# Kernel optimization log

Measured on AMD Instinct MI355X. Metric: run time of the kernel, lower is better.

Reference implementation:

```python
import jax, jax.numpy as jnp
import numpy as np
import math

B, S, D, H = 2, 2048, 1024, 16
HD = D // H  # head_dim = 64
NEG = -1.0e9


def _xavier(key, shape, gain):
    fan_in, fan_out = shape[1], shape[0]
    bound = gain * math.sqrt(6.0 / (fan_in + fan_out))
    return jax.random.uniform(key, shape, jnp.float32, -bound, bound)


def setup_inputs() -> dict:
    key = jax.random.key(0)
    ks = jax.random.split(key, 7)
    gain = 1.0 / math.sqrt(2.0)
    q = jax.random.normal(ks[0], (B, S, D), jnp.float32)
    pad_mask = jax.random.randint(ks[1], (B, S), 0, 2) > 0  # True = masked key
    # ensure not all keys masked per row
    pad_mask = pad_mask.at[:, 0].set(False)
    Wq = _xavier(ks[2], (D, D), gain)
    Wk = _xavier(ks[3], (D, D), gain)
    Wv = _xavier(ks[4], (D, D), gain)
    Wo = _xavier(ks[5], (D, D), gain)
    bk = jax.random.normal(ks[6], (4, D), jnp.float32) * 0.02
    return {"q": q, "pad_mask": pad_mask,
            "Wq": Wq, "bq": bk[0], "Wk": Wk, "bk": bk[1],
            "Wv": Wv, "bv": bk[2], "Wo": Wo, "bo": bk[3]}


def reference(q, pad_mask, Wq, bq, Wk, bk, Wv, bv, Wo, bo):
    # Self-attention: k = v = q (k, v args are None in this config)
    x = q
    # torch Linear: y = x @ W.T + b
    qh = (x @ Wq.T + bq).reshape(B, S, H, HD).transpose(0, 2, 1, 3)  # [B,H,S,HD]
    kh = (x @ Wk.T + bk).reshape(B, S, H, HD).transpose(0, 2, 1, 3)
    vh = (x @ Wv.T + bv).reshape(B, S, H, HD).transpose(0, 2, 1, 3)

    scores = jnp.einsum('bhqd,bhkd->bhqk', qh, kh) / math.sqrt(HD)  # [B,H,S,S]
    causal = jnp.triu(jnp.ones((S, S), bool), k=1)                  # [S,S]
    scores = jnp.where(causal[None, None], NEG, scores)
    scores = jnp.where(pad_mask[:, None, None, :], NEG, scores)

    probs = jax.nn.softmax(scores, axis=-1)
    out = jnp.einsum('bhqk,bhkd->bhqd', probs, vh)                  # [B,H,S,HD]
    out = out.transpose(0, 2, 1, 3).reshape(B, S, D)
    return out @ Wo.T + bo
```

## Files before the change

kernel.cpp:

```cpp
#include <hip/hip_runtime.h>
#include <hip/hip_bf16.h>

#define BB 2
#define SS 2048
#define DD 1024
#define HH 16
#define HD 64
#define MM (BB * SS)
#define NQKV 3072

typedef __attribute__((ext_vector_type(8))) short short8;
typedef __attribute__((ext_vector_type(4))) short s16x4;
typedef __attribute__((ext_vector_type(4))) float floatx4;
typedef __attribute__((ext_vector_type(4))) float f32x4;
using bf16 = __hip_bfloat16;

__device__ __forceinline__ float b2f(bf16 x) { return __bfloat162float(x); }
__device__ __forceinline__ short f2bs(float x) {
    bf16 h = __float2bfloat16(x);
    return *reinterpret_cast<short*>(&h);
}
__device__ __forceinline__ float bs2f(short s) {
    bf16 h; *reinterpret_cast<short*>(&h) = s; return __bfloat162float(h);
}

__device__ __forceinline__ int lds_off(int row, int chunk) {
    return row * 64 + ((chunk ^ (row & 7)) * 8);
}

#define GL16(gp, lp)                                                        \
    __builtin_amdgcn_global_load_lds(                                       \
        (const __attribute__((address_space(1))) void*)(gp),                \
        (__attribute__((address_space(3))) void*)(lp), 16, 0, 0)

#define N_WCAT (NQKV * DD / 4)
#define N_X    (MM * DD / 4)
#define N_WOB  (DD * DD / 4)

__global__ __launch_bounds__(256) void convert_all(
    const float* __restrict__ Wq, const float* __restrict__ Wk,
    const float* __restrict__ Wv, const float* __restrict__ X,
    const float* __restrict__ Wo,
    short* __restrict__ wcat, short* __restrict__ xb, short* wob)
{
    const int total = N_WCAT + N_X + (wob ? N_WOB : 0);
    const int stride = gridDim.x * blockDim.x;
    for (int i = blockIdx.x * blockDim.x + threadIdx.x; i < total; i += stride) {
        f32x4 v; short* dp;
        if (i < N_WCAT) {
            const int e = i * 4;
            const int z = e >> 20;
            const int off = e & 0xFFFFF;
            const float* src = (z == 0) ? Wq : (z == 1) ? Wk : Wv;
            v = *(const f32x4*)(src + off);
            dp = wcat + e;
        } else if (i < N_WCAT + N_X) {
            const int e = (i - N_WCAT) * 4;
            v = *(const f32x4*)(X + e);
            dp = xb + e;
        } else {
            const int e = (i - N_WCAT - N_X) * 4;
            v = *(const f32x4*)(Wo + e);
            dp = wob + e;
        }
        s16x4 o; o[0] = f2bs(v[0]); o[1] = f2bs(v[1]); o[2] = f2bs(v[2]); o[3] = f2bs(v[3]);
        *(s16x4*)dp = o;
    }
}

__global__ __launch_bounds__(256) void convert_w(
    const float* __restrict__ W, short* __restrict__ dst)
{
    const int stride = gridDim.x * blockDim.x;
    for (int i = blockIdx.x * blockDim.x + threadIdx.x; i < DD * DD / 4; i += stride) {
        f32x4 v = *(const f32x4*)(W + i * 4);
        s16x4 o; o[0] = f2bs(v[0]); o[1] = f2bs(v[1]); o[2] = f2bs(v[2]); o[3] = f2bs(v[3]);
        *(s16x4*)(dst + i * 4) = o;
    }
}

__global__ __launch_bounds__(256, 6) void qkv_gemm2(
    const short* __restrict__ Xb, const short* __restrict__ Wcat,
    const float* __restrict__ bq, const float* __restrict__ bk, const float* __restrict__ bv,
    bf16* __restrict__ outQ, bf16* __restrict__ outK, bf16* __restrict__ outV)
{
    __shared__ short As[128 * 64];
    __shared__ short Bs[64 * 64];

    const int tid  = threadIdx.x;
    const int lane = tid & 63;
    const int wave = tid >> 6;
    const int wm   = wave & 1;
    const int wn   = wave >> 1;
    const int g    = lane >> 4;
    const int fr   = lane & 15;

    const int m0 = blockIdx.x * 128;
    const int n0 = blockIdx.y * 64;

    const int l8  = lane >> 3;
    const int sch = (lane & 7) ^ l8;
    const short* agl = Xb   + (size_t)(m0 + l8) * DD + sch * 8;
    const short* bgl = Wcat + (size_t)(n0 + l8) * DD + sch * 8;

    floatx4 acc[4][2];
#pragma unroll
    for (int i = 0; i < 4; ++i)
#pragma unroll
        for (int j = 0; j < 2; ++j) acc[i][j] = (floatx4){0.f, 0.f, 0.f, 0.f};

    for (int kb = 0; kb < DD; kb += 64) {
        __syncthreads();
#pragma unroll
        for (int j = 0; j < 4; ++j) {
            const int r = wave * 32 + j * 8;
            GL16(agl + (size_t)r * DD + kb, &As[r * 64]);
        }
#pragma unroll
        for (int j = 0; j < 2; ++j) {
            const int r = wave * 16 + j * 8;
            GL16(bgl + (size_t)r * DD + kb, &Bs[r * 64]);
        }
        __syncthreads();

#pragma unroll
        for (int kk = 0; kk < 2; ++kk) {
            const int kc = kk * 4 + g;
            short8 af[4], bf[2];
#pragma unroll
            for (int t = 0; t < 4; ++t)
                af[t] = *(const short8*)&As[lds_off(wm * 64 + t * 16 + fr, kc)];
#pragma unroll
            for (int u = 0; u < 2; ++u)
                bf[u] = *(const short8*)&Bs[lds_off(wn * 32 + u * 16 + fr, kc)];
#pragma unroll
            for (int mt = 0; mt < 4; ++mt)
#pragma unroll
                for (int nt = 0; nt < 2; ++nt)
                    acc[mt][nt] = __builtin_amdgcn_mfma_f32_16x16x32_bf16(
                        af[mt], bf[nt], acc[mt][nt], 0, 0, 0);
        }
    }

#pragma unroll
    for (int nt = 0; nt < 2; ++nt) {
        const int n  = n0 + wn * 32 + nt * 16 + fr;
        const int z  = n >> 10;
        const int nn = n & 1023;
        const int h_ = nn >> 6;
        const int d_ = nn & 63;
        const float biasv = ((z == 0) ? bq : (z == 1) ? bk : bv)[nn];
        bf16* outp = (z == 0) ? outQ : (z == 1) ? outK : outV;
#pragma unroll
        for (int mt = 0; mt < 4; ++mt) {
#pragma unroll
            for (int reg = 0; reg < 4; ++reg) {
                const int m  = m0 + wm * 64 + mt * 16 + g * 4 + reg;
                const int b_ = m >> 11;
                const int s_ = m & (SS - 1);
                const float v = acc[mt][nt][reg] + biasv;
                size_t off;
                if (z == 2) off = ((size_t)((b_ * HH + h_) * HD + d_)) * SS + s_;
                else        off = ((size_t)((b_ * HH + h_) * SS + s_)) * HD + d_;
                outp[off] = __float2bfloat16(v);
            }
        }
    }
}

__global__ __launch_bounds__(256, 6) void o_gemm2(
    const short* __restrict__ A, const short* __restrict__ Wob,
    const float* __restrict__ bias, float* __restrict__ out)
{
    __shared__ short As[128 * 64];
    __shared__ short Bs[64 * 64];

    const int tid  = threadIdx.x;
    const int lane = tid & 63;
    const int wave = tid >> 6;
    const int wm   = wave & 1;
    const int wn   = wave >> 1;
    const int g    = lane >> 4;
    const int fr   = lane & 15;

    const int m0 = blockIdx.x * 128;
    const int n0 = blockIdx.y * 64;

    const int l8  = lane >> 3;
    const int sch = (lane & 7) ^ l8;
    const short* agl = A   + (size_t)(m0 + l8) * DD + sch * 8;
    const short* bgl = Wob + (size_t)(n0 + l8) * DD + sch * 8;

    floatx4 acc[4][2];
#pragma unroll
    for (int i = 0; i < 4; ++i)
#pragma unroll
        for (int j = 0; j < 2; ++j) acc[i][j] = (floatx4){0.f, 0.f, 0.f, 0.f};

    for (int kb = 0; kb < DD; kb += 64) {
        __syncthreads();
#pragma unroll
        for (int j = 0; j < 4; ++j) {
            const int r = wave * 32 + j * 8;
            GL16(agl + (size_t)r * DD + kb, &As[r * 64]);
        }
#pragma unroll
        for (int j = 0; j < 2; ++j) {
            const int r = wave * 16 + j * 8;
            GL16(bgl + (size_t)r * DD + kb, &Bs[r * 64]);
        }
        __syncthreads();

#pragma unroll
        for (int kk = 0; kk < 2; ++kk) {
            const int kc = kk * 4 + g;
            short8 af[4], bf[2];
#pragma unroll
            for (int t = 0; t < 4; ++t)
                af[t] = *(const short8*)&As[lds_off(wm * 64 + t * 16 + fr, kc)];
#pragma unroll
            for (int u = 0; u < 2; ++u)
                bf[u] = *(const short8*)&Bs[lds_off(wn * 32 + u * 16 + fr, kc)];
#pragma unroll
            for (int mt = 0; mt < 4; ++mt)
#pragma unroll
                for (int nt = 0; nt < 2; ++nt)
                    acc[mt][nt] = __builtin_amdgcn_mfma_f32_16x16x32_bf16(
                        af[mt], bf[nt], acc[mt][nt], 0, 0, 0);
        }
    }

#pragma unroll
    for (int nt = 0; nt < 2; ++nt) {
        const int n = n0 + wn * 32 + nt * 16 + fr;
        const float biasv = bias[n];
#pragma unroll
        for (int mt = 0; mt < 4; ++mt) {
#pragma unroll
            for (int reg = 0; reg < 4; ++reg) {
                const int m = m0 + wm * 64 + mt * 16 + g * 4 + reg;
                out[(size_t)m * DD + n] = acc[mt][nt][reg] + biasv;
            }
        }
    }
}

__global__ __launch_bounds__(256) void flash_mfma7(
    const bf16* __restrict__ Qh,
    const bf16* __restrict__ Kh,
    const bf16* __restrict__ VT,
    const int*  __restrict__ pad,
    bf16* __restrict__ attn)
{
    __shared__ short Ks[2][64 * 64];
    __shared__ short Vs[2][64 * 64];
    __shared__ short Pld[4][16 * 64];

    const int tid  = threadIdx.x;
    const int lane = tid & 63;
    const int wave = tid >> 6;
    const int xcd = blockIdx.x & 7;
    const int idx = blockIdx.x >> 3;
    const int bh  = (xcd << 2) | (idx & 3);
    const int qt  = 31 - (idx >> 2);
    const int q0  = qt * 64 + wave * 16;
    const int b_  = bh >> 4;
    const int h_  = bh & 15;

    const int g  = lane >> 4;
    const int fr = lane & 15;
    const int k8 = g * 8;

    short* myP = Pld[wave];

    const bf16* qbase = Qh + ((size_t)bh * SS + q0 + fr) * HD + k8;
    short8 qf[2];
#pragma unroll
    for (int hh = 0; hh < 2; ++hh) {
        short8 rawq = *(const short8*)((const short*)qbase + hh * 32);
#pragma unroll
        for (int j = 0; j < 8; ++j) qf[hh][j] = f2bs(bs2f(rawq[j]) * 0.125f);
    }

    const int* padrow = pad + b_ * SS;
    const short* kbh = (const short*)(Kh + (size_t)bh * SS * HD);
    const short* vbh = (const short*)(VT + (size_t)bh * HD * SS);

    const int l8  = lane >> 3;
    const int sch = (lane & 7) ^ l8;
    auto stageKV = [&](int buf, int kb) {
#pragma unroll
        for (int j = 0; j < 2; ++j) {
            const int r = wave * 16 + j * 8;
            GL16(kbh + (size_t)(kb + r + l8) * HD + sch * 8, &Ks[buf][r * 64]);
            GL16(vbh + (size_t)(r + l8) * SS + kb + sch * 8, &Vs[buf][r * 64]);
        }
    };

    floatx4 o[4] = {{0,0,0,0},{0,0,0,0},{0,0,0,0},{0,0,0,0}};
    float l_acc[4] = {0.f, 0.f, 0.f, 0.f};

    const int kend = qt * 64 + 63;

    stageKV(0, 0);
    asm volatile("s_waitcnt vmcnt(0)" ::: "memory");
    __syncthreads();

    for (int kb = 0; kb <= kend; kb += 64) {
        const int cur = (kb >> 6) & 1;
        if (kb + 64 <= kend) stageKV(cur ^ 1, kb + 64);

        const short* Kc = Ks[cur];
        const short* Vc = Vs[cur];

        floatx4 c[4];
        __builtin_amdgcn_s_setprio(1);
#pragma unroll
        for (int t = 0; t < 4; ++t) {
            short8 kf0 = *(const short8*)&Kc[(t * 16 + fr) * 64 + ((g       ^ (fr & 7)) << 3)];
            short8 kf1 = *(const short8*)&Kc[(t * 16 + fr) * 64 + (((g + 4) ^ (fr & 7)) << 3)];
            floatx4 cc = {0, 0, 0, 0};
            cc = __builtin_amdgcn_mfma_f32_16x16x32_bf16(qf[0], kf0, cc, 0, 0, 0);
            cc = __builtin_amdgcn_mfma_f32_16x16x32_bf16(qf[1], kf1, cc, 0, 0, 0);
            c[t] = cc;
        }
        __builtin_amdgcn_s_setprio(0);

        bool pm[4];
#pragma unroll
        for (int t = 0; t < 4; ++t) pm[t] = (padrow[kb + t * 16 + fr] != 0);

#pragma unroll
        for (int reg = 0; reg < 4; ++reg) {
            const int q   = q0 + g * 4 + reg;
            const int row = g * 4 + reg;
#pragma unroll
            for (int t = 0; t < 4; ++t) {
                const int key = kb + t * 16 + fr;
                const float p = (key <= q && !pm[t]) ? __expf(c[t][reg]) : 0.f;
                l_acc[reg] += p;
                const int col = t * 16 + fr;
                myP[row * 64 + (((col >> 3) ^ (row & 7)) << 3) + (col & 7)] = f2bs(p);
            }
        }

        short8 pf0 = *(const short8*)&myP[fr * 64 + ((g       ^ (fr & 7)) << 3)];
        short8 pf1 = *(const short8*)&myP[fr * 64 + (((g + 4) ^ (fr & 7)) << 3)];
        __builtin_amdgcn_s_setprio(1);
#pragma unroll
        for (int n = 0; n < 4; ++n) {
            short8 vf0 = *(const short8*)&Vc[(n * 16 + fr) * 64 + ((g       ^ (fr & 7)) << 3)];
            short8 vf1 = *(const short8*)&Vc[(n * 16 + fr) * 64 + (((g + 4) ^ (fr & 7)) << 3)];
            o[n] = __builtin_amdgcn_mfma_f32_16x16x32_bf16(pf0, vf0, o[n], 0, 0, 0);
            o[n] = __builtin_amdgcn_mfma_f32_16x16x32_bf16(pf1, vf1, o[n], 0, 0, 0);
        }
        __builtin_amdgcn_s_setprio(0);

        asm volatile("s_waitcnt vmcnt(0)" ::: "memory");
        __syncthreads();
    }

    float inv[4];
#pragma unroll
    for (int reg = 0; reg < 4; ++reg) {
        float l = l_acc[reg];
#pragma unroll
        for (int off = 1; off < 16; off <<= 1) l += __shfl_xor(l, off);
        inv[reg] = 1.f / fmaxf(l, 1e-38f);
    }
#pragma unroll
    for (int n = 0; n < 4; ++n) {
#pragma unroll
        for (int reg = 0; reg < 4; ++reg) {
            const int q = q0 + g * 4 + reg;
            attn[((size_t)(b_ * SS + q)) * DD + h_ * HD + n * 16 + fr] =
                __float2bfloat16(o[n][reg] * inv[reg]);
        }
    }
}

extern "C" void kernel_launch(void* const* d_in, const int* in_sizes, int n_in,
                              void* d_out, int out_size, void* d_ws, size_t ws_size,
                              hipStream_t stream) {
    const float* x   = (const float*)d_in[0];
    const int*   pad = (const int*)  d_in[1];
    const float* Wq  = (const float*)d_in[2];
    const float* bq  = (const float*)d_in[3];
    const float* Wk  = (const float*)d_in[4];
    const float* bk  = (const float*)d_in[5];
    const float* Wv  = (const float*)d_in[6];
    const float* bv  = (const float*)d_in[7];
    const float* Wo  = (const float*)d_in[8];
    const float* bo  = (const float*)d_in[9];
    float* out = (float*)d_out;

    const size_t NELEM = (size_t)BB * HH * SS * HD;
    bf16* Qh   = (bf16*)d_ws;
    bf16* Kh   = Qh + NELEM;
    bf16* VT   = Kh + NELEM;
    bf16* attn = VT + NELEM;
    short* Wcat = (short*)d_out;
    short* Xb   = (short*)d_out + (size_t)NQKV * DD;

    const size_t ws_need = 4 * NELEM * sizeof(bf16) + (size_t)DD * DD * sizeof(short);
    const bool big_ws = ws_size >= ws_need;
    short* Wob = big_ws ? (short*)(attn + NELEM) : (short*)Qh;

    convert_all<<<2048, 256, 0, stream>>>(Wq, Wk, Wv, x, Wo, Wcat, Xb,
                                          big_ws ? Wob : nullptr);

    dim3 gq(MM / 128, NQKV / 64);
    qkv_gemm2<<<gq, 256, 0, stream>>>(Xb, Wcat, bq, bk, bv, Qh, Kh, VT);

    flash_mfma7<<<BB * HH * 32, 256, 0, stream>>>(Qh, Kh, VT, pad, attn);

    if (!big_ws) convert_w<<<512, 256, 0, stream>>>(Wo, Wob);

    dim3 go(MM / 128, DD / 64);
    o_gemm2<<<go, 256, 0, stream>>>((const short*)attn, Wob, bo, out);
}
```

Measured before the change: 200.3 us.

## Compact unmasked keys and values so attention skips padded keys

```diff
diff --git a/kernel.cpp b/kernel.cpp
--- a/kernel.cpp
+++ b/kernel.cpp
@@ -79,10 +79,45 @@
     }
 }
 
+__global__ __launch_bounds__(256) void build_idx(
+    const int* __restrict__ pad, int* __restrict__ cidx, int* __restrict__ pfx)
+{
+    const int b   = blockIdx.x;
+    const int tid = threadIdx.x;
+    __shared__ int part[256];
+    const int* pr = pad + b * SS;
+    int* ci = cidx + b * SS;
+    int* pf = pfx + b * SS;
+
+    const int s0 = tid * 8;
+    int loc[8]; int sum = 0;
+#pragma unroll
+    for (int j = 0; j < 8; ++j) { loc[j] = (pr[s0 + j] == 0) ? 1 : 0; sum += loc[j]; }
+    part[tid] = sum;
+    __syncthreads();
+    for (int off = 1; off < 256; off <<= 1) {
+        const int v   = part[tid];
+        const int add = (tid >= off) ? part[tid - off] : 0;
+        __syncthreads();
+        part[tid] = v + add;
+        __syncthreads();
+    }
+    int run = (tid > 0) ? part[tid - 1] : 0;
+#pragma unroll
+    for (int j = 0; j < 8; ++j) {
+        run += loc[j];
+        pf[s0 + j] = run;
+        if (loc[j]) ci[run - 1] = s0 + j;
+    }
+    const int total = part[255];
+    for (int j = total + tid; j < SS; j += 256) ci[j] = SS;
+}
+
 __global__ __launch_bounds__(256, 6) void qkv_gemm2(
     const short* __restrict__ Xb, const short* __restrict__ Wcat,
     const float* __restrict__ bq, const float* __restrict__ bk, const float* __restrict__ bv,
-    bf16* __restrict__ outQ, bf16* __restrict__ outK, bf16* __restrict__ outV)
+    const int* __restrict__ pad, const int* __restrict__ pfx,
+    bf16* __restrict__ outQ, bf16* __restrict__ outKc, bf16* __restrict__ outVTc)
 {
     __shared__ short As[128 * 64];
     __shared__ short Bs[64 * 64];
@@ -150,7 +185,6 @@
         const int h_ = nn >> 6;
         const int d_ = nn & 63;
         const float biasv = ((z == 0) ? bq : (z == 1) ? bk : bv)[nn];
-        bf16* outp = (z == 0) ? outQ : (z == 1) ? outK : outV;
 #pragma unroll
         for (int mt = 0; mt < 4; ++mt) {
 #pragma unroll
@@ -159,10 +193,18 @@
                 const int b_ = m >> 11;
                 const int s_ = m & (SS - 1);
                 const float v = acc[mt][nt][reg] + biasv;
-                size_t off;
-                if (z == 2) off = ((size_t)((b_ * HH + h_) * HD + d_)) * SS + s_;
-                else        off = ((size_t)((b_ * HH + h_) * SS + s_)) * HD + d_;
-                outp[off] = __float2bfloat16(v);
+                if (z == 0) {
+                    outQ[((size_t)((b_ * HH + h_) * SS + s_)) * HD + d_] =
+                        __float2bfloat16(v);
+                } else if (pad[b_ * SS + s_] == 0) {
+                    const int cs = pfx[b_ * SS + s_] - 1;
+                    if (z == 1)
+                        outKc[((size_t)((b_ * HH + h_) * SS + cs)) * HD + d_] =
+                            __float2bfloat16(v);
+                    else
+                        outVTc[((size_t)((b_ * HH + h_) * HD + d_)) * SS + cs] =
+                            __float2bfloat16(v);
+                }
             }
         }
     }
@@ -245,11 +287,12 @@
     }
 }
 
-__global__ __launch_bounds__(256) void flash_mfma7(
+__global__ __launch_bounds__(256) void flash_mfma9(
     const bf16* __restrict__ Qh,
-    const bf16* __restrict__ Kh,
-    const bf16* __restrict__ VT,
-    const int*  __restrict__ pad,
+    const bf16* __restrict__ Kc,
+    const bf16* __restrict__ VTc,
+    const int*  __restrict__ cidx,
+    const int*  __restrict__ pfx,
     bf16* __restrict__ attn)
 {
     __shared__ short Ks[2][64 * 64];
@@ -282,9 +325,10 @@
         for (int j = 0; j < 8; ++j) qf[hh][j] = f2bs(bs2f(rawq[j]) * 0.125f);
     }
 
-    const int* padrow = pad + b_ * SS;
-    const short* kbh = (const short*)(Kh + (size_t)bh * SS * HD);
-    const short* vbh = (const short*)(VT + (size_t)bh * HD * SS);
+    const int* corow = cidx + b_ * SS;
+    const int nkeys  = pfx[b_ * SS + qt * 64 + 63];
+    const short* kbh = (const short*)(Kc  + (size_t)bh * SS * HD);
+    const short* vbh = (const short*)(VTc + (size_t)bh * HD * SS);
 
     const int l8  = lane >> 3;
     const int sch = (lane & 7) ^ l8;
@@ -300,25 +344,23 @@
     floatx4 o[4] = {{0,0,0,0},{0,0,0,0},{0,0,0,0},{0,0,0,0}};
     float l_acc[4] = {0.f, 0.f, 0.f, 0.f};
 
-    const int kend = qt * 64 + 63;
-
     stageKV(0, 0);
     asm volatile("s_waitcnt vmcnt(0)" ::: "memory");
     __syncthreads();
 
-    for (int kb = 0; kb <= kend; kb += 64) {
+    for (int kb = 0; kb < nkeys; kb += 64) {
         const int cur = (kb >> 6) & 1;
-        if (kb + 64 <= kend) stageKV(cur ^ 1, kb + 64);
-
-        const short* Kc = Ks[cur];
+        if (kb + 64 < nkeys) stageKV(cur ^ 1, kb + 64);
+
+        const short* Kt = Ks[cur];
         const short* Vc = Vs[cur];
 
         floatx4 c[4];
         __builtin_amdgcn_s_setprio(1);
 #pragma unroll
         for (int t = 0; t < 4; ++t) {
-            short8 kf0 = *(const short8*)&Kc[(t * 16 + fr) * 64 + ((g       ^ (fr & 7)) << 3)];
-            short8 kf1 = *(const short8*)&Kc[(t * 16 + fr) * 64 + (((g + 4) ^ (fr & 7)) << 3)];
+            short8 kf0 = *(const short8*)&Kt[(t * 16 + fr) * 64 + ((g       ^ (fr & 7)) << 3)];
+            short8 kf1 = *(const short8*)&Kt[(t * 16 + fr) * 64 + (((g + 4) ^ (fr & 7)) << 3)];
             floatx4 cc = {0, 0, 0, 0};
             cc = __builtin_amdgcn_mfma_f32_16x16x32_bf16(qf[0], kf0, cc, 0, 0, 0);
             cc = __builtin_amdgcn_mfma_f32_16x16x32_bf16(qf[1], kf1, cc, 0, 0, 0);
@@ -326,9 +368,9 @@
         }
         __builtin_amdgcn_s_setprio(0);
 
-        bool pm[4];
-#pragma unroll
-        for (int t = 0; t < 4; ++t) pm[t] = (padrow[kb + t * 16 + fr] != 0);
+        int ko[4];
+#pragma unroll
+        for (int t = 0; t < 4; ++t) ko[t] = corow[kb + t * 16 + fr];
 
 #pragma unroll
         for (int reg = 0; reg < 4; ++reg) {
@@ -336,8 +378,7 @@
             const int row = g * 4 + reg;
 #pragma unroll
             for (int t = 0; t < 4; ++t) {
-                const int key = kb + t * 16 + fr;
-                const float p = (key <= q && !pm[t]) ? __expf(c[t][reg]) : 0.f;
+                const float p = (ko[t] <= q) ? __expf(c[t][reg]) : 0.f;
                 l_acc[reg] += p;
                 const int col = t * 16 + fr;
                 myP[row * 64 + (((col >> 3) ^ (row & 7)) << 3) + (col & 7)] = f2bs(p);
@@ -396,23 +437,31 @@
 
     const size_t NELEM = (size_t)BB * HH * SS * HD;
     bf16* Qh   = (bf16*)d_ws;
-    bf16* Kh   = Qh + NELEM;
-    bf16* VT   = Kh + NELEM;
-    bf16* attn = VT + NELEM;
+    bf16* Kc   = Qh + NELEM;
+    bf16* VTc  = Kc + NELEM;
+    bf16* attn = VTc + NELEM;
+    int*  cidx = (int*)(attn + NELEM);
+    int*  pfx  = cidx + BB * SS;
     short* Wcat = (short*)d_out;
     short* Xb   = (short*)d_out + (size_t)NQKV * DD;
 
-    const size_t ws_need = 4 * NELEM * sizeof(bf16) + (size_t)DD * DD * sizeof(short);
+    const size_t ws_need = 4 * NELEM * sizeof(bf16) + 2 * (size_t)BB * SS * sizeof(int)
+                         + (size_t)DD * DD * sizeof(short);
     const bool big_ws = ws_size >= ws_need;
-    short* Wob = big_ws ? (short*)(attn + NELEM) : (short*)Qh;
+    short* Wob = big_ws ? (short*)(pfx + BB * SS) : (short*)Qh;
 
     convert_all<<<2048, 256, 0, stream>>>(Wq, Wk, Wv, x, Wo, Wcat, Xb,
                                           big_ws ? Wob : nullptr);
 
+    build_idx<<<BB, 256, 0, stream>>>(pad, cidx, pfx);
+
+    hipMemsetAsync(Kc, 0, 2 * NELEM * sizeof(bf16), stream);
+
     dim3 gq(MM / 128, NQKV / 64);
-    qkv_gemm2<<<gq, 256, 0, stream>>>(Xb, Wcat, bq, bk, bv, Qh, Kh, VT);
-
-    flash_mfma7<<<BB * HH * 32, 256, 0, stream>>>(Qh, Kh, VT, pad, attn);
+    qkv_gemm2<<<gq, 256, 0, stream>>>(Xb, Wcat, bq, bk, bv, pad, pfx,
+                                      Qh, Kc, VTc);
+
+    flash_mfma9<<<BB * HH * 32, 256, 0, stream>>>(Qh, Kc, VTc, cidx, pfx, attn);
 
     if (!big_ws) convert_w<<<512, 256, 0, stream>>>(Wo, Wob);
 
```

Result: faster. 189.4 us (-5.4%).
